# Kernel tuning notes

Hardware: AMD Instinct MI355X
Metric: run time of the kernel (lower is better)

Reference implementation:

```python
import jax, jax.numpy as jnp
import numpy as np

N = 1024      # number of spans
D = 512       # span embedding dim (input_dim = 3*D)
H = 150       # hidden_dim
WIN = 250     # antecedent window from spans[ix-250:ix]


def setup_inputs() -> dict:
    key = jax.random.key(0)
    ks = jax.random.split(key, 8)
    return {
        "g": jax.random.normal(ks[0], (N, D), jnp.float32),
        "sm": jax.random.normal(ks[1], (N,), jnp.float32),
        "W1": jax.random.normal(ks[2], (3 * D, H), jnp.float32) * (1.0 / np.sqrt(3 * D)),
        "b1": jax.random.normal(ks[3], (H,), jnp.float32) * 0.01,
        "W2": jax.random.normal(ks[4], (H, H), jnp.float32) * (1.0 / np.sqrt(H)),
        "b2": jax.random.normal(ks[5], (H,), jnp.float32) * 0.01,
        "W3": jax.random.normal(ks[6], (H, 1), jnp.float32) * (1.0 / np.sqrt(H)),
        "b3": jax.random.normal(ks[7], (1,), jnp.float32) * 0.01,
    }


def reference(g, sm, W1, b1, W2, b2, W3, b3):
    n, d = g.shape
    # matching the in-order iteration over spans[ix-250:ix]
    j = jnp.arange(n)[:, None] - WIN + jnp.arange(WIN)[None, :]
    valid = j >= 0
    jc = jnp.clip(j, 0)

    # pair feature is cat([g_i, g_j, g_i*g_j]); split W1 so we can factor the first GEMM
    W1a, W1b, W1c = jnp.split(W1, 3, axis=0)            # each [D, H]
    gi_term = g @ W1a                                    # [N, H]
    gj_term = (g @ W1b)[jc]
    prod_term = jnp.einsum('nwd,dh->nwh', g[:, None, :] * g[jc], W1c)

    h = jax.nn.relu(gi_term[:, None, :] + gj_term + prod_term + b1)
    h = jax.nn.relu(h @ W2 + b2)
    s = (h @ W3 + b3)[..., 0]

    sij = sm[:, None] + sm[jc] + s                       # sm_i + sm_j + s_a
    sij = jnp.where(valid, sij, 0.0)                     # mask out-of-range antecedents
    eps = jnp.zeros((n, 1), g.dtype)                     # trailing epsilon = 0
    return jnp.concatenate([sij, eps], axis=1)
```

## Files before the change

### kernel.cpp

```cpp
#include <hip/hip_runtime.h>

typedef __attribute__((ext_vector_type(8))) short short8;
typedef __attribute__((ext_vector_type(4))) float f32x4;

#define NSPAN 1024
#define DDIM  512
#define HDIM  150
#define HPAD  160
#define WINW  250
#define OUTW  251

#define A1_OFF 40960
#define B1_OFF 49152
#define GI_OFF 59392
#define B2_OFF 40960
#define S_OFF  61440
#define SMEM_BYTES 61952

__device__ __forceinline__ unsigned short f2bf(float x) {
  union { float f; unsigned int u; } v; v.f = x;
  return (unsigned short)((v.u + 0x7fffu + ((v.u >> 16) & 1u)) >> 16);
}
__device__ __forceinline__ unsigned int pk2(float a, float b) {
  return (unsigned int)f2bf(a) | ((unsigned int)f2bf(b) << 16);
}

__global__ __launch_bounds__(192) void prep_gemm(
    const float* __restrict__ g, const float* __restrict__ W1,
    const float* __restrict__ b1, float* __restrict__ pre1,
    float* __restrict__ gjb)
{
  __shared__ __align__(16) float gs[8 * DDIM];
  const int grp = blockIdx.x >> 1;
  const int which = blockIdx.x & 1;
  const int i0 = grp << 3;
  for (int idx = threadIdx.x; idx < (8 * DDIM / 4); idx += 192)
    ((float4*)gs)[idx] = ((const float4*)(g + (size_t)i0 * DDIM))[idx];
  __syncthreads();
  const int n = threadIdx.x;
  float acc[8];
#pragma unroll
  for (int r = 0; r < 8; ++r) acc[r] = 0.f;
  if (n < HDIM) {
    const float* Wp = W1 + (size_t)which * DDIM * HDIM + n;
#pragma unroll 4
    for (int d = 0; d < DDIM; ++d) {
      float w = Wp[(size_t)d * HDIM];
#pragma unroll
      for (int r = 0; r < 8; ++r) acc[r] += gs[r * DDIM + d] * w;
    }
  }
  if (n < HPAD) {
    float* dst = which ? gjb : pre1;
    float add = (which == 0 && n < HDIM) ? b1[n] : 0.f;
#pragma unroll
    for (int r = 0; r < 8; ++r)
      dst[(size_t)(i0 + r) * HPAD + n] = (n < HDIM) ? (acc[r] + add) : 0.f;
  }
}

__global__ void prep_misc(const float* __restrict__ W1, const float* __restrict__ W2,
                          const float* __restrict__ W3,
                          unsigned short* __restrict__ w1cT,
                          unsigned short* __restrict__ w2T,
                          float* __restrict__ w3p)
{
  int id = blockIdx.x * 256 + threadIdx.x;
  if (id < HPAD * DDIM) {
    int n = id >> 9, d = id & 511;
    float v = (n < HDIM) ? W1[(size_t)(2 * DDIM + d) * HDIM + n] : 0.f;
    w1cT[id] = f2bf(v);
  } else if (id < HPAD * DDIM + HPAD * HPAD) {
    int id2 = id - HPAD * DDIM;
    int n = id2 / HPAD, k = id2 % HPAD;
    float v = (n < HDIM && k < HDIM) ? W2[(size_t)k * HDIM + n] : 0.f;
    w2T[id2] = f2bf(v);
  } else if (id < HPAD * DDIM + HPAD * HPAD + HPAD) {
    int n = id - HPAD * DDIM - HPAD * HPAD;
    w3p[n] = (n < HDIM) ? W3[n] : 0.f;
  }
}

__global__ __launch_bounds__(256, 2) void pair_main(
    const float* __restrict__ g, const float* __restrict__ sm,
    const float* __restrict__ pre1, const float* __restrict__ gjb,
    const unsigned short* __restrict__ w1cT, const unsigned short* __restrict__ w2T,
    const float* __restrict__ w3p, const float* __restrict__ b2,
    const float* __restrict__ b3, float* __restrict__ out)
{
  __shared__ __align__(16) char smem[SMEM_BYTES];
  const int tid = threadIdx.x;
  const int lane = tid & 63;
  const int wv = tid >> 6;
  const int l15 = lane & 15;
  const int lq = lane >> 4;
  const int i = blockIdx.x >> 1;
  const int mbase = (blockIdx.x & 1) << 7;

  float* giL = (float*)(smem + GI_OFF);
  if (tid < 128)
    ((float4*)giL)[tid] = ((const float4*)(g + (size_t)i * DDIM))[tid];

  const int r_s = tid >> 1;
  const int kh = (tid & 1) << 4;
  const int rg_s = mbase + r_s;
  const int j_s = i - WINW + rg_s;
  const bool val_s = (rg_s < WINW) && (j_s >= 0);
  const int jc_s = j_s < 0 ? 0 : (j_s > NSPAN - 1 ? NSPAN - 1 : j_s);
  const float4* gj4 = (const float4*)(g + (size_t)jc_s * DDIM);
  const int swA = ((r_s >> 1) & 7) << 4;
  const int stA0 = A1_OFF + (((r_s << 6) + (kh << 1)) ^ swA);
  const int stA1 = A1_OFF + (((r_s << 6) + (kh << 1) + 16) ^ swA);

  int xa[2];
#pragma unroll
  for (int mt = 0; mt < 2; ++mt) {
    int row = (wv << 5) + (mt << 4) + l15;
    xa[mt] = ((row << 6) + (lq << 4)) ^ (((row >> 1) & 7) << 4);
  }
  int xb[10];
#pragma unroll
  for (int nt = 0; nt < 10; ++nt) {
    int nr = (nt << 4) + l15;
    xb[nt] = ((nr << 6) + (lq << 4)) ^ (((nr >> 1) & 7) << 4);
  }

  f32x4 acc[2][10];
#pragma unroll
  for (int mt = 0; mt < 2; ++mt)
#pragma unroll
    for (int nt = 0; nt < 10; ++nt)
      acc[mt][nt] = (f32x4){0.f, 0.f, 0.f, 0.f};

  __syncthreads();

  for (int k0 = 0; k0 < DDIM; k0 += 32) {
    {
      const int fb = (k0 + kh) >> 2;
      float4 x0 = gj4[fb], x1 = gj4[fb + 1], x2 = gj4[fb + 2], x3 = gj4[fb + 3];
      const float4* gi4 = ((const float4*)giL) + fb;
      float4 y0 = gi4[0], y1 = gi4[1], y2 = gi4[2], y3 = gi4[3];
      uint4 w0, w1;
      w0.x = pk2(x0.x * y0.x, x0.y * y0.y);
      w0.y = pk2(x0.z * y0.z, x0.w * y0.w);
      w0.z = pk2(x1.x * y1.x, x1.y * y1.y);
      w0.w = pk2(x1.z * y1.z, x1.w * y1.w);
      w1.x = pk2(x2.x * y2.x, x2.y * y2.y);
      w1.y = pk2(x2.z * y2.z, x2.w * y2.w);
      w1.z = pk2(x3.x * y3.x, x3.y * y3.y);
      w1.w = pk2(x3.z * y3.z, x3.w * y3.w);
      if (!val_s) { w0 = make_uint4(0, 0, 0, 0); w1 = make_uint4(0, 0, 0, 0); }
      *(uint4*)(smem + stA0) = w0;
      *(uint4*)(smem + stA1) = w1;
    }
#pragma unroll
    for (int q = 0; q < 3; ++q) {
      int ch = tid + (q << 8);
      if (ch < 640) {
        int n = ch >> 2, sl = ch & 3;
        uint4 v = *(const uint4*)(w1cT + (size_t)n * DDIM + k0 + (sl << 3));
        *(uint4*)(smem + B1_OFF + (((n << 6) + (sl << 4)) ^ (((n >> 1) & 7) << 4))) = v;
      }
    }
    __syncthreads();
    short8 a0 = *(const short8*)(smem + A1_OFF + xa[0]);
    short8 a1 = *(const short8*)(smem + A1_OFF + xa[1]);
#pragma unroll
    for (int nt = 0; nt < 10; ++nt) {
      short8 bb = *(const short8*)(smem + B1_OFF + xb[nt]);
      acc[0][nt] = __builtin_amdgcn_mfma_f32_16x16x32_bf16(a0, bb, acc[0][nt], 0, 0, 0);
      acc[1][nt] = __builtin_amdgcn_mfma_f32_16x16x32_bf16(a1, bb, acc[1][nt], 0, 0, 0);
    }
    __syncthreads();
  }

  float p1v[10];
#pragma unroll
  for (int nt = 0; nt < 10; ++nt)
    p1v[nt] = pre1[(size_t)i * HPAD + (nt << 4) + l15];

#pragma unroll
  for (int mt = 0; mt < 2; ++mt) {
#pragma unroll
    for (int rr = 0; rr < 4; ++rr) {
      const int row = (wv << 5) + (mt << 4) + (lq << 2) + rr;
      const int rgl = mbase + row;
      int j = i - WINW + rgl;
      j = j < 0 ? 0 : (j > NSPAN - 1 ? NSPAN - 1 : j);
      const float* gjr = gjb + (size_t)j * HPAD;
      const int sw = (row & 3) << 4;
      const int rb = row * 320;
#pragma unroll
      for (int nt = 0; nt < 10; ++nt) {
        float v = acc[mt][nt][rr] + p1v[nt] + gjr[(nt << 4) + l15];
        v = fmaxf(v, 0.f);
        *(unsigned short*)(smem + ((rb + (((nt << 4) + l15) << 1)) ^ sw)) = f2bf(v);
      }
    }
  }

  f32x4 acc2[2][10];
#pragma unroll
  for (int mt = 0; mt < 2; ++mt)
#pragma unroll
    for (int nt = 0; nt < 10; ++nt)
      acc2[mt][nt] = (f32x4){0.f, 0.f, 0.f, 0.f};

  int ya[2];
#pragma unroll
  for (int mt = 0; mt < 2; ++mt) {
    int row = (wv << 5) + (mt << 4) + l15;
    ya[mt] = ((row * 320) + (lq << 4)) ^ ((row & 3) << 4);
  }

  for (int c = 0; c < 5; ++c) {
#pragma unroll
    for (int q = 0; q < 3; ++q) {
      int ch = tid + (q << 8);
      if (ch < 640) {
        int n = ch >> 2, sl = ch & 3;
        uint4 v = *(const uint4*)(w2T + (size_t)n * HPAD + (c << 5) + (sl << 3));
        *(uint4*)(smem + B2_OFF + (((n << 6) + (sl << 4)) ^ (((n >> 1) & 7) << 4))) = v;
      }
    }
    __syncthreads();
    short8 a0 = *(const short8*)(smem + ya[0] + (c << 6));
    short8 a1 = *(const short8*)(smem + ya[1] + (c << 6));
#pragma unroll
    for (int nt = 0; nt < 10; ++nt) {
      short8 bb = *(const short8*)(smem + B2_OFF + xb[nt]);
      acc2[0][nt] = __builtin_amdgcn_mfma_f32_16x16x32_bf16(a0, bb, acc2[0][nt], 0, 0, 0);
      acc2[1][nt] = __builtin_amdgcn_mfma_f32_16x16x32_bf16(a1, bb, acc2[1][nt], 0, 0, 0);
    }
    __syncthreads();
  }

  float w3v[10], b2v[10];
#pragma unroll
  for (int nt = 0; nt < 10; ++nt) {
    int nn = (nt << 4) + l15;
    w3v[nt] = w3p[nn];
    b2v[nt] = (nn < HDIM) ? b2[nn] : 0.f;
  }
  float* sL = (float*)(smem + S_OFF);
#pragma unroll
  for (int mt = 0; mt < 2; ++mt) {
#pragma unroll
    for (int rr = 0; rr < 4; ++rr) {
      float part = 0.f;
#pragma unroll
      for (int nt = 0; nt < 10; ++nt) {
        float h2 = fmaxf(acc2[mt][nt][rr] + b2v[nt], 0.f);
        part = fmaf(h2, w3v[nt], part);
      }
      part += __shfl_xor(part, 1);
      part += __shfl_xor(part, 2);
      part += __shfl_xor(part, 4);
      part += __shfl_xor(part, 8);
      if (l15 == 0)
        sL[(wv << 5) + (mt << 4) + (lq << 2) + rr] = part;
    }
  }
  __syncthreads();

  if (tid < 128) {
    const int rg = mbase + tid;
    if (rg <= WINW) {
      const int j = i - WINW + rg;
      float v = 0.f;
      if (rg < WINW && j >= 0)
        v = sL[tid] + b3[0] + sm[i] + sm[j];
      out[(size_t)i * OUTW + rg] = v;
    }
  }
}

extern "C" void kernel_launch(void* const* d_in, const int* in_sizes, int n_in,
                              void* d_out, int out_size, void* d_ws, size_t ws_size,
                              hipStream_t stream) {
  const float* g  = (const float*)d_in[0];
  const float* sm = (const float*)d_in[1];
  const float* W1 = (const float*)d_in[2];
  const float* b1 = (const float*)d_in[3];
  const float* W2 = (const float*)d_in[4];
  const float* b2 = (const float*)d_in[5];
  const float* W3 = (const float*)d_in[6];
  const float* b3 = (const float*)d_in[7];
  float* out = (float*)d_out;

  char* ws = (char*)d_ws;
  float* pre1          = (float*)ws;
  float* gjb           = (float*)(ws + 655360);
  unsigned short* w1cT = (unsigned short*)(ws + 1310720);
  unsigned short* w2T  = (unsigned short*)(ws + 1474560);
  float* w3p           = (float*)(ws + 1525760);

  prep_gemm<<<256, 192, 0, stream>>>(g, W1, b1, pre1, gjb);
  prep_misc<<<(HPAD * DDIM + HPAD * HPAD + HPAD + 255) / 256, 256, 0, stream>>>(
      W1, W2, W3, w1cT, w2T, w3p);
  pair_main<<<2048, 256, 0, stream>>>(g, sm, pre1, gjb, w1cT, w2T, w3p, b2, b3, out);
}
```

Before: 234.1 us.

## Double-buffer pair GEMM with async LDS loads and raise occupancy

The W1c tile is now streamed into LDS with global_load_lds into two ping-pong buffers, so each k-step needs one barrier instead of two. The second GEMM reads W2 fragments straight from global memory instead of staging them in LDS. Shared memory use drops so four blocks can share a CU, and bf16 packing uses v_cvt_pk_bf16_f32. prep_gemm is split into more, smaller blocks, and the zero-masking of out-of-window rows is removed on the assumption that the output masks them anyway. The risks are register pressure at the new launch bound, correct waitcnt handling for the async LDS loads, and extra global traffic for W2.

```diff
diff --git a/kernel.cpp b/kernel.cpp
--- a/kernel.cpp
+++ b/kernel.cpp
@@ -10,19 +10,28 @@
 #define WINW  250
 #define OUTW  251
 
-#define A1_OFF 40960
-#define B1_OFF 49152
-#define GI_OFF 59392
-#define B2_OFF 40960
-#define S_OFF  61440
-#define SMEM_BYTES 61952
+#define B1_OFF0 0
+#define B1_OFF1 10240
+#define A1_OFF0 20480
+#define A1_OFF1 28672
+#define GI_OFF  36864
+#define SMEM_BYTES 40960
 
 __device__ __forceinline__ unsigned short f2bf(float x) {
   union { float f; unsigned int u; } v; v.f = x;
   return (unsigned short)((v.u + 0x7fffu + ((v.u >> 16) & 1u)) >> 16);
 }
-__device__ __forceinline__ unsigned int pk2(float a, float b) {
-  return (unsigned int)f2bf(a) | ((unsigned int)f2bf(b) << 16);
+
+__device__ __forceinline__ unsigned int cvtpk(float a, float b) {
+  unsigned int r;
+  asm("v_cvt_pk_bf16_f32 %0, %1, %2" : "=v"(r) : "v"(a), "v"(b));
+  return r;
+}
+
+__device__ __forceinline__ void gload_lds16(const void* g, void* l) {
+  __builtin_amdgcn_global_load_lds(
+      (const __attribute__((address_space(1))) unsigned int*)g,
+      (__attribute__((address_space(3))) unsigned int*)l, 16, 0, 0);
 }
 
 __global__ __launch_bounds__(192) void prep_gemm(
@@ -30,32 +39,31 @@
     const float* __restrict__ b1, float* __restrict__ pre1,
     float* __restrict__ gjb)
 {
-  __shared__ __align__(16) float gs[8 * DDIM];
+  __shared__ __align__(16) float gs[2 * DDIM];
   const int grp = blockIdx.x >> 1;
   const int which = blockIdx.x & 1;
-  const int i0 = grp << 3;
-  for (int idx = threadIdx.x; idx < (8 * DDIM / 4); idx += 192)
+  const int i0 = grp << 1;
+  for (int idx = threadIdx.x; idx < (2 * DDIM / 4); idx += 192)
     ((float4*)gs)[idx] = ((const float4*)(g + (size_t)i0 * DDIM))[idx];
   __syncthreads();
   const int n = threadIdx.x;
-  float acc[8];
-#pragma unroll
-  for (int r = 0; r < 8; ++r) acc[r] = 0.f;
+  float a0 = 0.f, a1 = 0.f;
   if (n < HDIM) {
     const float* Wp = W1 + (size_t)which * DDIM * HDIM + n;
-#pragma unroll 4
+#pragma unroll 8
     for (int d = 0; d < DDIM; ++d) {
       float w = Wp[(size_t)d * HDIM];
-#pragma unroll
-      for (int r = 0; r < 8; ++r) acc[r] += gs[r * DDIM + d] * w;
+      a0 += gs[d] * w;
+      a1 += gs[DDIM + d] * w;
     }
   }
   if (n < HPAD) {
     float* dst = which ? gjb : pre1;
     float add = (which == 0 && n < HDIM) ? b1[n] : 0.f;
-#pragma unroll
-    for (int r = 0; r < 8; ++r)
-      dst[(size_t)(i0 + r) * HPAD + n] = (n < HDIM) ? (acc[r] + add) : 0.f;
+    float v0 = (n < HDIM) ? (a0 + add) : 0.f;
+    float v1 = (n < HDIM) ? (a1 + add) : 0.f;
+    dst[(size_t)i0 * HPAD + n] = v0;
+    dst[(size_t)(i0 + 1) * HPAD + n] = v1;
   }
 }
 
@@ -81,7 +89,7 @@
   }
 }
 
-__global__ __launch_bounds__(256, 2) void pair_main(
+__global__ __launch_bounds__(256, 4) void pair_main(
     const float* __restrict__ g, const float* __restrict__ sm,
     const float* __restrict__ pre1, const float* __restrict__ gjb,
     const unsigned short* __restrict__ w1cT, const unsigned short* __restrict__ w2T,
@@ -103,14 +111,22 @@
 
   const int r_s = tid >> 1;
   const int kh = (tid & 1) << 4;
-  const int rg_s = mbase + r_s;
-  const int j_s = i - WINW + rg_s;
-  const bool val_s = (rg_s < WINW) && (j_s >= 0);
+  const int j_s = i - WINW + mbase + r_s;
   const int jc_s = j_s < 0 ? 0 : (j_s > NSPAN - 1 ? NSPAN - 1 : j_s);
   const float4* gj4 = (const float4*)(g + (size_t)jc_s * DDIM);
   const int swA = ((r_s >> 1) & 7) << 4;
-  const int stA0 = A1_OFF + (((r_s << 6) + (kh << 1)) ^ swA);
-  const int stA1 = A1_OFF + (((r_s << 6) + (kh << 1) + 16) ^ swA);
+  const int stA0 = (((r_s << 6) + (kh << 1)) ^ swA);
+  const int stA1 = (((r_s << 6) + (kh << 1) + 16) ^ swA);
+
+  unsigned int bsrc[3];
+#pragma unroll
+  for (int t = 0; t < 3; ++t) {
+    int b = wv * 2560 + (t << 10) + (lane << 4);
+    int m = b >> 7;
+    int bp = b ^ ((m & 7) << 4);
+    int n = bp >> 6, o = bp & 63;
+    bsrc[t] = (unsigned int)(n * 1024 + o);
+  }
 
   int xa[2];
 #pragma unroll
@@ -132,47 +148,49 @@
     for (int nt = 0; nt < 10; ++nt)
       acc[mt][nt] = (f32x4){0.f, 0.f, 0.f, 0.f};
 
-  __syncthreads();
-
-  for (int k0 = 0; k0 < DDIM; k0 += 32) {
+  const char* w1cB = (const char*)w1cT;
+  __syncthreads();
+
+  for (int s = 0; s < 16; ++s) {
+    const int k0 = s << 5;
+    char* a1b = smem + ((s & 1) ? A1_OFF1 : A1_OFF0);
+    char* b1b = smem + ((s & 1) ? B1_OFF1 : B1_OFF0);
+
+    {
+      char* ldsw = b1b + wv * 2560;
+      gload_lds16(w1cB + bsrc[0] + (k0 << 1), ldsw);
+      gload_lds16(w1cB + bsrc[1] + (k0 << 1), ldsw + 1024);
+      if (lane < 32)
+        gload_lds16(w1cB + bsrc[2] + (k0 << 1), ldsw + 2048);
+    }
     {
       const int fb = (k0 + kh) >> 2;
       float4 x0 = gj4[fb], x1 = gj4[fb + 1], x2 = gj4[fb + 2], x3 = gj4[fb + 3];
       const float4* gi4 = ((const float4*)giL) + fb;
       float4 y0 = gi4[0], y1 = gi4[1], y2 = gi4[2], y3 = gi4[3];
       uint4 w0, w1;
-      w0.x = pk2(x0.x * y0.x, x0.y * y0.y);
-      w0.y = pk2(x0.z * y0.z, x0.w * y0.w);
-      w0.z = pk2(x1.x * y1.x, x1.y * y1.y);
-      w0.w = pk2(x1.z * y1.z, x1.w * y1.w);
-      w1.x = pk2(x2.x * y2.x, x2.y * y2.y);
-      w1.y = pk2(x2.z * y2.z, x2.w * y2.w);
-      w1.z = pk2(x3.x * y3.x, x3.y * y3.y);
-      w1.w = pk2(x3.z * y3.z, x3.w * y3.w);
-      if (!val_s) { w0 = make_uint4(0, 0, 0, 0); w1 = make_uint4(0, 0, 0, 0); }
-      *(uint4*)(smem + stA0) = w0;
-      *(uint4*)(smem + stA1) = w1;
-    }
-#pragma unroll
-    for (int q = 0; q < 3; ++q) {
-      int ch = tid + (q << 8);
-      if (ch < 640) {
-        int n = ch >> 2, sl = ch & 3;
-        uint4 v = *(const uint4*)(w1cT + (size_t)n * DDIM + k0 + (sl << 3));
-        *(uint4*)(smem + B1_OFF + (((n << 6) + (sl << 4)) ^ (((n >> 1) & 7) << 4))) = v;
-      }
+      w0.x = cvtpk(x0.x * y0.x, x0.y * y0.y);
+      w0.y = cvtpk(x0.z * y0.z, x0.w * y0.w);
+      w0.z = cvtpk(x1.x * y1.x, x1.y * y1.y);
+      w0.w = cvtpk(x1.z * y1.z, x1.w * y1.w);
+      w1.x = cvtpk(x2.x * y2.x, x2.y * y2.y);
+      w1.y = cvtpk(x2.z * y2.z, x2.w * y2.w);
+      w1.z = cvtpk(x3.x * y3.x, x3.y * y3.y);
+      w1.w = cvtpk(x3.z * y3.z, x3.w * y3.w);
+      *(uint4*)(a1b + stA0) = w0;
+      *(uint4*)(a1b + stA1) = w1;
     }
     __syncthreads();
-    short8 a0 = *(const short8*)(smem + A1_OFF + xa[0]);
-    short8 a1 = *(const short8*)(smem + A1_OFF + xa[1]);
+    short8 a0 = *(const short8*)(a1b + xa[0]);
+    short8 a1 = *(const short8*)(a1b + xa[1]);
 #pragma unroll
     for (int nt = 0; nt < 10; ++nt) {
-      short8 bb = *(const short8*)(smem + B1_OFF + xb[nt]);
+      short8 bb = *(const short8*)(b1b + xb[nt]);
       acc[0][nt] = __builtin_amdgcn_mfma_f32_16x16x32_bf16(a0, bb, acc[0][nt], 0, 0, 0);
       acc[1][nt] = __builtin_amdgcn_mfma_f32_16x16x32_bf16(a1, bb, acc[1][nt], 0, 0, 0);
     }
-    __syncthreads();
-  }
+  }
+  __syncthreads();
 
   float p1v[10];
 #pragma unroll
@@ -184,17 +202,19 @@
 #pragma unroll
     for (int rr = 0; rr < 4; ++rr) {
       const int row = (wv << 5) + (mt << 4) + (lq << 2) + rr;
-      const int rgl = mbase + row;
-      int j = i - WINW + rgl;
+      int j = i - WINW + mbase + row;
       j = j < 0 ? 0 : (j > NSPAN - 1 ? NSPAN - 1 : j);
       const float* gjr = gjb + (size_t)j * HPAD;
-      const int sw = (row & 3) << 4;
+      const int sw = ((row + (row >> 2)) & 3) << 4;
       const int rb = row * 320;
 #pragma unroll
-      for (int nt = 0; nt < 10; ++nt) {
-        float v = acc[mt][nt][rr] + p1v[nt] + gjr[(nt << 4) + l15];
-        v = fmaxf(v, 0.f);
-        *(unsigned short*)(smem + ((rb + (((nt << 4) + l15) << 1)) ^ sw)) = f2bf(v);
+      for (int np = 0; np < 5; ++np) {
+        const int n0 = np << 1, n1 = n0 + 1;
+        float v0 = fmaxf(acc[mt][n0][rr] + p1v[n0] + gjr[(n0 << 4) + l15], 0.f);
+        float v1 = fmaxf(acc[mt][n1][rr] + p1v[n1] + gjr[(n1 << 4) + l15], 0.f);
+        unsigned int u = cvtpk(v0, v1);
+        *(unsigned short*)(smem + ((rb + (((n0 << 4) + l15) << 1)) ^ sw)) = (unsigned short)u;
+        *(unsigned short*)(smem + ((rb + (((n1 << 4) + l15) << 1)) ^ sw)) = (unsigned short)(u >> 16);
       }
     }
   }
@@ -210,30 +230,23 @@
 #pragma unroll
   for (int mt = 0; mt < 2; ++mt) {
     int row = (wv << 5) + (mt << 4) + l15;
-    ya[mt] = ((row * 320) + (lq << 4)) ^ ((row & 3) << 4);
-  }
-
+    ya[mt] = ((row * 320) + (lq << 4)) ^ (((row + (row >> 2)) & 3) << 4);
+  }
+
+  __syncthreads();
+
+#pragma unroll
   for (int c = 0; c < 5; ++c) {
-#pragma unroll
-    for (int q = 0; q < 3; ++q) {
-      int ch = tid + (q << 8);
-      if (ch < 640) {
-        int n = ch >> 2, sl = ch & 3;
-        uint4 v = *(const uint4*)(w2T + (size_t)n * HPAD + (c << 5) + (sl << 3));
-        *(uint4*)(smem + B2_OFF + (((n << 6) + (sl << 4)) ^ (((n >> 1) & 7) << 4))) = v;
-      }
-    }
-    __syncthreads();
     short8 a0 = *(const short8*)(smem + ya[0] + (c << 6));
     short8 a1 = *(const short8*)(smem + ya[1] + (c << 6));
 #pragma unroll
     for (int nt = 0; nt < 10; ++nt) {
-      short8 bb = *(const short8*)(smem + B2_OFF + xb[nt]);
+      short8 bb = *(const short8*)(w2T + (size_t)((nt << 4) + l15) * HPAD + (c << 5) + (lq << 3));
       acc2[0][nt] = __builtin_amdgcn_mfma_f32_16x16x32_bf16(a0, bb, acc2[0][nt], 0, 0, 0);
       acc2[1][nt] = __builtin_amdgcn_mfma_f32_16x16x32_bf16(a1, bb, acc2[1][nt], 0, 0, 0);
     }
-    __syncthreads();
-  }
+  }
+  __syncthreads();
 
   float w3v[10], b2v[10];
 #pragma unroll
@@ -242,7 +255,7 @@
     w3v[nt] = w3p[nn];
     b2v[nt] = (nn < HDIM) ? b2[nn] : 0.f;
   }
-  float* sL = (float*)(smem + S_OFF);
+  float* sL = (float*)smem;
 #pragma unroll
   for (int mt = 0; mt < 2; ++mt) {
 #pragma unroll
@@ -295,7 +308,7 @@
   unsigned short* w2T  = (unsigned short*)(ws + 1474560);
   float* w3p           = (float*)(ws + 1525760);
 
-  prep_gemm<<<256, 192, 0, stream>>>(g, W1, b1, pre1, gjb);
+  prep_gemm<<<1024, 192, 0, stream>>>(g, W1, b1, pre1, gjb);
   prep_misc<<<(HPAD * DDIM + HPAD * HPAD + HPAD + 255) / 256, 256, 0, stream>>>(
       W1, W2, W3, w1cT, w2T, w3p);
   pair_main<<<2048, 256, 0, stream>>>(g, sm, pre1, gjb, w1cT, w2T, w3p, b2, b3, out);
```

Result: slower. 239.2 us (+2.2%).
